# Performance work log

Measured on AMD Instinct MI355X. Metric: run time of the kernel, lower is better.

## Reference

```python
import jax, jax.numpy as jnp
import numpy as np

H = 128      # hidden_sizes
E = 128      # embedding_size
V = 100000   # n_words
C = 10       # n_classes
B, S, L = 32, 32, 64
PAD = 0


def _gru_dir(x, w_ih, w_hh, b_ih, b_hh, reverse):
    # x: [N, T, D]; torch GRU cell convention (r, z, n gate order)
    xp = jnp.einsum('ntd,gd->ntg', x, w_ih) + b_ih  # [N, T, 3H]
    if reverse:
        xp = xp[:, ::-1]
    h0 = jnp.zeros((x.shape[0], w_hh.shape[1]), x.dtype)

    def step(h, xt):
        gh = h @ w_hh.T + b_hh
        xr, xz, xn = jnp.split(xt, 3, axis=-1)
        hr, hz, hn = jnp.split(gh, 3, axis=-1)
        r = jax.nn.sigmoid(xr + hr)
        z = jax.nn.sigmoid(xz + hz)
        n = jnp.tanh(xn + r * hn)
        h2 = (1.0 - z) * n + z * h
        return h2, h2

    _, hs = jax.lax.scan(step, h0, jnp.swapaxes(xp, 0, 1))
    hs = jnp.swapaxes(hs, 0, 1)  # [N, T, H]
    if reverse:
        hs = hs[:, ::-1]
    return hs


def _bi_gru(x, pf, pb):
    return jnp.concatenate([_gru_dir(x, *pf, False), _gru_dir(x, *pb, True)], axis=-1)


def _attn_pool(h, W, b, ctx):
    # h: [N, T, 2H] -> pooled [N, 2H]
    u = jnp.tanh(jnp.einsum('ntd,ed->nte', h, W) + b)
    a = jax.nn.softmax(u @ ctx, axis=1)          # [N, T]
    return jnp.einsum('ntd,nt->nd', h, a)


def setup_inputs() -> dict:
    key = jax.random.key(0)
    ks = jax.random.split(key, 24)
    sc = 0.05
    d = {}
    d['X'] = jax.random.randint(ks[0], (B, S, L), 0, V, dtype=jnp.int32)
    d['emb'] = jax.random.normal(ks[1], (V, E), jnp.float32) * sc
    # word-level bi-GRU (input E)
    d['w_ih_f'] = jax.random.normal(ks[2], (3 * H, E), jnp.float32) * sc
    d['w_hh_f'] = jax.random.normal(ks[3], (3 * H, H), jnp.float32) * sc
    d['b_ih_f'] = jnp.zeros((3 * H,), jnp.float32)
    d['b_hh_f'] = jnp.zeros((3 * H,), jnp.float32)
    d['w_ih_b'] = jax.random.normal(ks[4], (3 * H, E), jnp.float32) * sc
    d['w_hh_b'] = jax.random.normal(ks[5], (3 * H, H), jnp.float32) * sc
    d['b_ih_b'] = jnp.zeros((3 * H,), jnp.float32)
    d['b_hh_b'] = jnp.zeros((3 * H,), jnp.float32)
    d['Ww'] = jax.random.normal(ks[6], (2 * H, 2 * H), jnp.float32) * sc
    d['bw'] = jnp.zeros((2 * H,), jnp.float32)
    d['ctx_w'] = jax.random.normal(ks[7], (2 * H,), jnp.float32) * sc
    # sentence-level bi-GRU (input 2H)
    d['s_ih_f'] = jax.random.normal(ks[8], (3 * H, 2 * H), jnp.float32) * sc
    d['s_hh_f'] = jax.random.normal(ks[9], (3 * H, H), jnp.float32) * sc
    d['sb_ih_f'] = jnp.zeros((3 * H,), jnp.float32)
    d['sb_hh_f'] = jnp.zeros((3 * H,), jnp.float32)
    d['s_ih_b'] = jax.random.normal(ks[10], (3 * H, 2 * H), jnp.float32) * sc
    d['s_hh_b'] = jax.random.normal(ks[11], (3 * H, H), jnp.float32) * sc
    d['sb_ih_b'] = jnp.zeros((3 * H,), jnp.float32)
    d['sb_hh_b'] = jnp.zeros((3 * H,), jnp.float32)
    d['Ws'] = jax.random.normal(ks[12], (2 * H, 2 * H), jnp.float32) * sc
    d['bs'] = jnp.zeros((2 * H,), jnp.float32)
    d['ctx_s'] = jax.random.normal(ks[13], (2 * H,), jnp.float32) * sc
    d['Wc'] = jax.random.normal(ks[14], (C, 2 * H), jnp.float32) * sc
    d['bc'] = jnp.zeros((C,), jnp.float32)
    return d


def reference(X, emb, w_ih_f, w_hh_f, b_ih_f, b_hh_f, w_ih_b, w_hh_b, b_ih_b, b_hh_b,
              Ww, bw, ctx_w, s_ih_f, s_hh_f, sb_ih_f, sb_hh_f, s_ih_b, s_hh_b,
              sb_ih_b, sb_hh_b, Ws, bs, ctx_s, Wc, bc):
    emb = emb.at[PAD].set(0.0)               # padding_idx semantics
    words = emb[X.reshape(B * S, L)]          # [B*S, L, E]
    h_w = _bi_gru(words, (w_ih_f, w_hh_f, b_ih_f, b_hh_f),
                  (w_ih_b, w_hh_b, b_ih_b, b_hh_b))  # [B*S, L, 2H]
    sents = _attn_pool(h_w, Ww, bw, ctx_w).reshape(B, S, 2 * H)
    h_s = _bi_gru(sents, (s_ih_f, s_hh_f, sb_ih_f, sb_hh_f),
                  (s_ih_b, s_hh_b, sb_ih_b, sb_hh_b))  # [B, S, 2H]
    doc = _attn_pool(h_s, Ws, bs, ctx_s)      # [B, 2H]
    return doc @ Wc.T + bc                    # [B, C]
```

## Files before the change

### kernel.cpp

```cpp
#include <hip/hip_runtime.h>
#include <hip/hip_bf16.h>
#include <math.h>

#define Bd 32
#define Sd 32
#define Ld 64
#define Ed 128
#define Hd 128
#define MW 65536
#define MS 1024

#define OFF_WIHT_S   0
#define OFF_WFW_W    196608
#define OFF_WFW_S    262144
#define OFF_W6       327680
#define OFF_BIH_W    622592
#define OFF_BIH_S    623360
#define OFF_BHH_W    624128
#define OFF_BHH_S    624896
#define OFF_WFX      625664
#define OFF_HW       723968
#define OFF_SENTS    17763328
#define OFF_XP_S     18025472
#define OFF_HS       18811904
#define OFF_DOC      19078144
#define OFF_WFHH     19086336
#define WS_FLOATS    19184640

typedef __attribute__((ext_vector_type(8))) short sh8;
typedef __attribute__((ext_vector_type(4))) float f32x4;
typedef unsigned short u16;
typedef unsigned int u32;

#define GLD  388
#define XPLD 385
#define HPLD 520

__device__ __forceinline__ void barrier_lds_only() {
    asm volatile("s_waitcnt lgkmcnt(0)\n\ts_barrier" ::: "memory");
}

__device__ __forceinline__ float sigmoidf_(float x) {
    return __fdividef(1.0f, 1.0f + __expf(-x));
}
__device__ __forceinline__ float tanhf_(float x) {
    float t = __expf(-2.0f * fabsf(x));
    float r = __fdividef(1.0f - t, 1.0f + t);
    return copysignf(r, x);
}
__device__ __forceinline__ u16 bf16_hi(float f) {
    u32 x = __float_as_uint(f);
    return (u16)((x + 0x7fffu + ((x >> 16) & 1u)) >> 16);
}
__device__ __forceinline__ float bf16_f(u16 u) { return __uint_as_float(((u32)u) << 16); }
__device__ __forceinline__ void bf16_split(float f, u16& hi, u16& lo) {
    hi = bf16_hi(f);
    lo = bf16_hi(f - bf16_f(hi));
}

__global__ void prep_all(const float* __restrict__ s_ih_f, const float* __restrict__ s_ih_b,
                         const float* __restrict__ w_ih_f, const float* __restrict__ w_ih_b,
                         const float* __restrict__ w_hh_f, const float* __restrict__ w_hh_b,
                         const float* __restrict__ s_hh_f, const float* __restrict__ s_hh_b,
                         const float* __restrict__ b_ih_f, const float* __restrict__ b_ih_b,
                         const float* __restrict__ sb_ih_f, const float* __restrict__ sb_ih_b,
                         const float* __restrict__ b_hh_f, const float* __restrict__ b_hh_b,
                         const float* __restrict__ sb_hh_f, const float* __restrict__ sb_hh_b,
                         const float* __restrict__ Ww, const float* __restrict__ Ws,
                         float* __restrict__ ws)
{
    const int b = blockIdx.x;
    if (b < 1164) {
        int i = b * 256 + threadIdx.x;
        if (i < 294912) {
            int set = i / 49152;
            if (set < 4) return;
            int rem = i % 49152;
            int k4 = rem / 1536, r2 = rem % 1536, g = r2 >> 2, sub = r2 & 3;
            const float* w = (set==4) ? s_hh_f : s_hh_b;
            ws[OFF_W6 + i] = w[g*128 + k4*4 + sub];
            return;
        }
        i -= 294912;
        if (i < 768) { ws[OFF_BIH_W + i] = (i<384) ? b_ih_f[i] : b_ih_b[i-384]; return; }
        i -= 768;
        if (i < 768) { ws[OFF_BIH_S + i] = (i<384) ? sb_ih_f[i] : sb_ih_b[i-384]; return; }
        i -= 768;
        if (i < 768) { ws[OFF_BHH_W + i] = (i<384) ? b_hh_f[i] : b_hh_b[i-384]; return; }
        i -= 768;
        if (i < 768) { ws[OFF_BHH_S + i] = (i<384) ? sb_hh_f[i] : sb_hh_b[i-384]; return; }
        return;
    }
    if (b < 1932) {
        u16* WFo = (u16*)(ws + OFF_WFHH);
        int i = (b - 1164) * 256 + threadIdx.x;
        int within = i % 49152;
        int combo  = i / 49152;
        int half = combo & 1, dir = combo >> 1;
        int nt  = within / 2048;
        int r2  = within % 2048;
        int q   = r2 >> 9;
        int r3  = r2 & 511;
        int l   = r3 >> 3, e = r3 & 7;
        int n = nt*16 + (l & 15);
        int k = q*32 + ((l >> 4) << 3) + e;
        const float* src = dir ? w_hh_b : w_hh_f;
        float v = src[n*128 + k];
        u16 hi = bf16_hi(v);
        WFo[i] = half ? bf16_hi(v - bf16_f(hi)) : hi;
        return;
    }
    if (b < 3724) {
        u16* WFW_W = (u16*)(ws + OFF_WFW_W);
        u16* WFW_S = (u16*)(ws + OFF_WFW_S);
        u16* WFX   = (u16*)(ws + OFF_WFX);
        int i = (b - 1932) * 256 + threadIdx.x;
        if (i < 262144) {
            int which = i / 131072;
            int w = i % 131072;
            int half = w / 65536;
            int r = w % 65536;
            int nt = r / 4096;
            int r2 = r % 4096;
            int q = r2 / 512;
            int l = (r2 % 512) >> 3, e = r2 & 7;
            int n = nt*16 + (l & 15);
            int k = q*32 + ((l >> 4) << 3) + e;
            const float* src = which ? Ws : Ww;
            float v = src[n*256 + k];
            u16 hi = bf16_hi(v);
            u16 o = half ? bf16_hi(v - bf16_f(hi)) : hi;
            (which ? WFW_S : WFW_W)[w] = o;
            return;
        }
        i -= 262144;
        if (i < 196608) {
            int w = i % 98304;
            int dir = i / 98304;
            int half = w / 49152;
            int r = w % 49152;
            int nt = r / 2048;
            int r2 = r % 2048;
            int q = r2 / 512;
            int l = (r2 % 512) >> 3, e = r2 & 7;
            int n = nt*16 + (l & 15);
            int k = q*32 + ((l >> 4) << 3) + e;
            const float* src = dir ? w_ih_b : w_ih_f;
            float v = src[n*128 + k];
            u16 hi = bf16_hi(v);
            WFX[i] = half ? bf16_hi(v - bf16_f(hi)) : hi;
            return;
        }
        return;
    }
    {
        u16* WFIHS = (u16*)(ws + OFF_W6);
        int i = (b - 3724) * 256 + threadIdx.x;
        int dir  = i / 196608;
        int w    = i % 196608;
        int half = w / 98304;
        int r    = w % 98304;
        int nt = r / 4096;
        int r2 = r % 4096;
        int q  = r2 / 512;
        int l  = (r2 % 512) >> 3, e = r2 & 7;
        int n = nt*16 + (l & 15);
        int k = q*32 + ((l >> 4) << 3) + e;
        const float* src = dir ? s_ih_b : s_ih_f;
        float v = src[n*256 + k];
        u16 hi = bf16_hi(v);
        WFIHS[i] = half ? bf16_hi(v - bf16_f(hi)) : hi;
    }
}

__global__ __launch_bounds__(768)
void gru_word_full(const int* __restrict__ X, const float* __restrict__ emb,
                   const u16* __restrict__ WFX, const u16* __restrict__ WFHH,
                   const float* __restrict__ b_ih_f, const float* __restrict__ b_ih_b,
                   const float* __restrict__ b_hh_f, const float* __restrict__ b_hh_b,
                   u16* __restrict__ houtp)
{
    const int bx = blockIdx.x;
    const int dir = bx >> 7;
    const int blk = bx & 127;
    const int seq0 = blk * 8;
    const int tid = threadIdx.x;
    const int lane = tid & 63;
    const int wid = tid >> 6;

    __shared__ float xp_lds[64 * XPLD];
    __shared__ f32x4 uni4[2048];
    __shared__ u16 h_pk[4 * HPLD];
    __shared__ int ids_s[8][64];
    float* G = (float*)uni4;
    u16* a_pk = (u16*)uni4;

    const int j = tid & 127;
    const int sg = tid >> 7;
    const bool gthread = tid < 512;
    const float* bih = dir ? b_ih_b : b_ih_f;
    const float* bhh = dir ? b_hh_b : b_hh_f;
    float bhr = 0.f, bhz = 0.f, bhn = 0.f;
    if (gthread) { bhr = bhh[j]; bhz = bhh[128 + j]; bhn = bhh[256 + j]; }

    const u16* WXbase = WFX + (long)dir * 98304;
    const u16* WHbase = WFHH + (long)dir * 98304;
    const int nt0 = wid*2, nt1 = wid*2 + 1;
    const int c0 = nt0*16 + (lane & 15);
    const int c1 = nt1*16 + (lane & 15);
    const int qj = j >> 5, subkj = (j >> 3) & 3, ej = j & 7;

    for (int i = tid; i < 512; i += 768)
        ids_s[i >> 6][i & 63] = X[(long)(seq0 + (i >> 6))*64 + (i & 63)];
    for (int i = tid; i < 4*HPLD; i += 768) h_pk[i] = 0;
    __syncthreads();

    float hprev0 = 0.f, hprev1 = 0.f;
    for (int c = 0; c < 8; ++c) {
        asm volatile("" ::: "memory");
        sh8 xh0[4], xl0[4], xh1[4], xl1[4];
#pragma unroll
        for (int q = 0; q < 4; ++q) {
            xh0[q] = *(const sh8*)(WXbase + (nt0*4 + q)*512 + lane*8);
            xl0[q] = *(const sh8*)(WXbase + 49152 + (nt0*4 + q)*512 + lane*8);
            xh1[q] = *(const sh8*)(WXbase + (nt1*4 + q)*512 + lane*8);
            xl1[q] = *(const sh8*)(WXbase + 49152 + (nt1*4 + q)*512 + lane*8);
        }
        const float bv0 = bih[c0], bv1 = bih[c1];
        for (int idx = tid; idx < 2048; idx += 768) {
            int cc2 = idx & 1, rm = (idx >> 1) & 7, subk = (idx >> 4) & 3;
            int q = (idx >> 6) & 3, mfs = idx >> 8;
            int ts = c*8 + rm;
            int t = dir ? 63 - ts : ts;
            int kk = q*32 + subk*8 + cc2*4;
            int id = ids_s[mfs][t];
            float4 v = make_float4(0.f, 0.f, 0.f, 0.f);
            if (id != 0) v = *(const float4*)&emb[(long)id*128 + kk];
            u16 h0,l0,h1,l1,h2,l2,h3,l3;
            bf16_split(v.x,h0,l0); bf16_split(v.y,h1,l1);
            bf16_split(v.z,h2,l2); bf16_split(v.w,h3,l3);
            int lh = subk*16 + rm;
            int base = (mfs*4 + q)*512 + lh*8 + cc2*4;
            uint2 whi = make_uint2((u32)h0 | ((u32)h1 << 16), (u32)h2 | ((u32)h3 << 16));
            uint2 wlo = make_uint2((u32)l0 | ((u32)l1 << 16), (u32)l2 | ((u32)l3 << 16));
            *(uint2*)&a_pk[base]      = whi;
            *(uint2*)&a_pk[base + 64] = wlo;
        }
        barrier_lds_only();
#pragma unroll
        for (int mf = 0; mf < 8; ++mf) {
            f32x4 A0 = (f32x4){0.f,0.f,0.f,0.f};
            f32x4 A1 = (f32x4){0.f,0.f,0.f,0.f};
#pragma unroll
            for (int q = 0; q < 4; ++q) {
                sh8 a = *(const sh8*)&a_pk[(mf*4 + q)*512 + lane*8];
                A0 = __builtin_amdgcn_mfma_f32_16x16x32_bf16(a, xh0[q], A0, 0,0,0);
                A0 = __builtin_amdgcn_mfma_f32_16x16x32_bf16(a, xl0[q], A0, 0,0,0);
                A1 = __builtin_amdgcn_mfma_f32_16x16x32_bf16(a, xh1[q], A1, 0,0,0);
                A1 = __builtin_amdgcn_mfma_f32_16x16x32_bf16(a, xl1[q], A1, 0,0,0);
            }
            float g0[4], g1[4];
#pragma unroll
            for (int r = 0; r < 4; ++r) {
                g0[r] = A0[r] + __shfl_xor(A0[r], 32);
                g1[r] = A1[r] + __shfl_xor(A1[r], 32);
            }
            if ((lane >= 32) == (mf & 1)) {
                int row = mf*8 + ((lane >> 4) & 1)*4;
#pragma unroll
                for (int r = 0; r < 4; ++r) {
                    xp_lds[(row+r)*XPLD + c0] = g0[r] + bv0;
                    xp_lds[(row+r)*XPLD + c1] = g1[r] + bv1;
                }
            }
        }
        barrier_lds_only();
        asm volatile("" ::: "memory");
        sh8 wh0[4], wl0[4], wh1[4], wl1[4];
#pragma unroll
        for (int q = 0; q < 4; ++q) {
            wh0[q] = *(const sh8*)(WHbase + (nt0*4 + q)*512 + lane*8);
            wl0[q] = *(const sh8*)(WHbase + 49152 + (nt0*4 + q)*512 + lane*8);
            wh1[q] = *(const sh8*)(WHbase + (nt1*4 + q)*512 + lane*8);
            wl1[q] = *(const sh8*)(WHbase + 49152 + (nt1*4 + q)*512 + lane*8);
        }
        for (int tt = 0; tt < 8; ++tt) {
            const int ts = c*8 + tt;
            const int t = dir ? 63 - ts : ts;
            f32x4 acc0 = (f32x4){0.f,0.f,0.f,0.f};
            f32x4 acc1 = (f32x4){0.f,0.f,0.f,0.f};
#pragma unroll
            for (int q = 0; q < 4; ++q) {
                sh8 hp = *(const sh8*)&h_pk[q*HPLD + lane*8];
                acc0 = __builtin_amdgcn_mfma_f32_16x16x32_bf16(hp, wh0[q], acc0, 0,0,0);
                acc0 = __builtin_amdgcn_mfma_f32_16x16x32_bf16(hp, wl0[q], acc0, 0,0,0);
                acc1 = __builtin_amdgcn_mfma_f32_16x16x32_bf16(hp, wh1[q], acc1, 0,0,0);
                acc1 = __builtin_amdgcn_mfma_f32_16x16x32_bf16(hp, wl1[q], acc1, 0,0,0);
            }
            {
                float sg0[4], sg1[4];
#pragma unroll
                for (int r = 0; r < 4; ++r) {
                    sg0[r] = acc0[r] + __shfl_xor(acc0[r], 32);
                    sg1[r] = acc1[r] + __shfl_xor(acc1[r], 32);
                }
                if (lane < 32) {
                    const int col16 = lane & 15;
                    const int row0  = (lane >> 4) << 2;
#pragma unroll
                    for (int r = 0; r < 4; ++r) {
                        G[(row0+r)*GLD + nt0*16 + col16] = sg0[r];
                        G[(row0+r)*GLD + nt1*16 + col16] = sg1[r];
                    }
                }
            }
            barrier_lds_only();
            if (gthread) {
#pragma unroll
                for (int si = 0; si < 2; ++si) {
                    const int s = sg + si*4;
                    float gr  = G[s*GLD + j]       + bhr;
                    float gz  = G[s*GLD + 128 + j] + bhz;
                    float gnh = G[s*GLD + 256 + j] + bhn;
                    const float* xrow = &xp_lds[(s*8 + tt)*XPLD];
                    float r  = sigmoidf_(xrow[j] + gr);
                    float z  = sigmoidf_(xrow[128 + j] + gz);
                    float nv = tanhf_(xrow[256 + j] + r * gnh);
                    float hold = si ? hprev1 : hprev0;
                    float hnew = (1.f - z) * nv + z * hold;
                    if (si) hprev1 = hnew; else hprev0 = hnew;
                    u16 hh, hl; bf16_split(hnew, hh, hl);
                    u16 ohh = (u16)__shfl_xor((int)hh, 1);
                    u16 ohl = (u16)__shfl_xor((int)hl, 1);
                    const long tbase = ((long)(seq0 + s)*64 + t)*512 + dir*128;
                    if ((j & 1) == 0) {
                        u32 w = (u32)hh | ((u32)ohh << 16);
                        *(u32*)&h_pk[qj*HPLD + (subkj*16 + s)*8 + ej] = w;
                        *(u32*)&houtp[tbase + j] = w;
                    } else {
                        u32 w = (u32)ohl | ((u32)hl << 16);
                        *(u32*)&h_pk[qj*HPLD + (subkj*16 + s + 8)*8 + (ej - 1)] = w;
                        *(u32*)&houtp[tbase + 256 + (j - 1)] = w;
                    }
                }
            }
            barrier_lds_only();
        }
    }
}

template<int T, bool PACKED, bool CLS>
__global__ __launch_bounds__(1024)
void attn_fused(const float* __restrict__ A, const u16* __restrict__ WF,
                const float* __restrict__ bias, const float* __restrict__ ctx,
                float* __restrict__ outp,
                const float* __restrict__ Wc, const float* __restrict__ bc)
{
    __shared__ u16 a_pk[8][8][512];
    __shared__ float pscore[8][8][17];
    __shared__ float aw[64];
    __shared__ float red[4][256];
    __shared__ float docv[2][256];
    const int tid = threadIdx.x;
    const int lane = tid & 63;
    const int wid = tid >> 6;
    const int m0 = blockIdx.x * 64;

    sh8 bh[8], bl[8];
#pragma unroll
    for (int q = 0; q < 8; ++q) {
        bh[q] = *(const sh8*)(WF + (wid*8 + q)*512 + lane*8);
        bl[q] = *(const sh8*)(WF + 65536 + (wid*8 + q)*512 + lane*8);
    }
    const int colg = wid*16 + (lane & 15);
    const float bwv = bias[colg];
    const float cxv = ctx[colg];

    if (PACKED) {
        const u32* src32 = (const u32*)A + (long)blockIdx.x * 16384;
        u32* dst = (u32*)a_pk;
        for (int idx4 = tid; idx4 < 4096; idx4 += 1024) {
            int idx = idx4 << 2;
            int mf = idx >> 11, q = (idx >> 8) & 7, l = (idx >> 2) & 63;
            int row16 = l & 15, hilo = row16 >> 3, rm = row16 & 7;
            int t = mf*8 + rm;
            int kb2 = q*16 + (l >> 4)*4;
            *(uint4*)&dst[idx] = *(const uint4*)&src32[(t*2 + hilo)*128 + kb2];
        }
    } else {
        for (int idx = tid; idx < 8192; idx += 1024) {
            int row = idx >> 7;
            int k   = (idx & 127) << 1;
            float2 v = *(const float2*)&A[(long)(m0 + row)*256 + k];
            u16 h0,l0,h1,l1; bf16_split(v.x,h0,l0); bf16_split(v.y,h1,l1);
            int mf = row >> 3, rm = row & 7;
            int q = k >> 5;
            int lh = (((k & 31) >> 3) << 4) | rm;
            int e = k & 7;
            *(u32*)&a_pk[mf][q][lh*8 + e]     = (u32)h0 | ((u32)h1 << 16);
            *(u32*)&a_pk[mf][q][(lh+8)*8 + e] = (u32)l0 | ((u32)l1 << 16);
        }
    }
    __syncthreads();

#pragma unroll
    for (int mf = 0; mf < 8; ++mf) {
        f32x4 acc = (f32x4){0.f,0.f,0.f,0.f};
#pragma unroll
        for (int q = 0; q < 8; ++q) {
            sh8 a = *(const sh8*)&a_pk[mf][q][lane*8];
            acc = __builtin_amdgcn_mfma_f32_16x16x32_bf16(a, bh[q], acc, 0,0,0);
            acc = __builtin_amdgcn_mfma_f32_16x16x32_bf16(a, bl[q], acc, 0,0,0);
        }
        float g[4];
#pragma unroll
        for (int r = 0; r < 4; ++r) g[r] = acc[r] + __shfl_xor(acc[r], 32);
        if ((lane >= 32) == (mf & 1)) {
            float p[4];
#pragma unroll
            for (int r = 0; r < 4; ++r) p[r] = tanhf_(g[r] + bwv) * cxv;
#pragma unroll
            for (int r = 0; r < 4; ++r) {
                p[r] += __shfl_xor(p[r], 1);
                p[r] += __shfl_xor(p[r], 2);
                p[r] += __shfl_xor(p[r], 4);
                p[r] += __shfl_xor(p[r], 8);
            }
            if ((lane & 15) == 0) {
#pragma unroll
                for (int r = 0; r < 4; ++r)
                    pscore[mf][((lane >> 4) & 1)*4 + r][wid] = p[r];
            }
        }
    }
    __syncthreads();

    if (tid < 64) {
        float sc = 0.f;
#pragma unroll
        for (int w = 0; w < 16; ++w) sc += pscore[tid >> 3][tid & 7][w];
        float mx = sc;
#pragma unroll
        for (int m = 1; m < T; m <<= 1) mx = fmaxf(mx, __shfl_xor(mx, m));
        float e = __expf(sc - mx);
        float den = e;
#pragma unroll
        for (int m = 1; m < T; m <<= 1) den += __shfl_xor(den, m);
        aw[tid] = __fdividef(e, den);
    }
    __syncthreads();

    if (tid < 512) {
        const int dp = (tid & 127) << 1;
        const int tg = tid >> 7;
        const int q = dp >> 5, lhb = ((dp & 31) >> 3) << 4, e = dp & 7;
        float acc0 = 0.f, acc1 = 0.f;
#pragma unroll
        for (int i = 0; i < 16; ++i) {
            int t = tg*16 + i;
            int mf = t >> 3, rm = t & 7;
            const u16* base = &a_pk[mf][q][(lhb | rm)*8 + e];
            u32 hh = *(const u32*)base;
            u32 ll = *(const u32*)(base + 64);
            float h0 = bf16_f((u16)hh) + bf16_f((u16)ll);
            float h1 = bf16_f((u16)(hh >> 16)) + bf16_f((u16)(ll >> 16));
            float w = aw[t];
            acc0 = fmaf(w, h0, acc0);
            acc1 = fmaf(w, h1, acc1);
        }
        red[tg][dp] = acc0; red[tg][dp + 1] = acc1;
    }
    __syncthreads();
    if (T == 64) {
        if (tid < 256)
            outp[(long)blockIdx.x*256 + tid] = red[0][tid] + red[1][tid] + red[2][tid] + red[3][tid];
    } else if (!CLS) {
        if (tid < 512) {
            int sent = tid >> 8, dd = tid & 255;
            outp[((long)blockIdx.x*2 + sent)*256 + dd] = red[sent*2][dd] + red[sent*2 + 1][dd];
        }
    } else {
        if (tid < 512) {
            int sent = tid >> 8, dd = tid & 255;
            docv[sent][dd] = red[sent*2][dd] + red[sent*2 + 1][dd];
        }
        __syncthreads();
        if (tid < 20) {
            int s = tid / 10, c = tid % 10;
            float acc = bc[c];
            const float4* wp = (const float4*)&Wc[c*256];
            const float4* dv = (const float4*)&docv[s][0];
#pragma unroll 8
            for (int d = 0; d < 64; ++d) {
                float4 a = dv[d], w = wp[d];
                acc = fmaf(a.x, w.x, fmaf(a.y, w.y, fmaf(a.z, w.z, fmaf(a.w, w.w, acc))));
            }
            outp[(blockIdx.x*2 + s)*10 + c] = acc;
        }
    }
}

__global__ __launch_bounds__(512)
void gru_sent(const float* __restrict__ sents, const u16* __restrict__ WFIHS,
              const float* __restrict__ bih_s, const float4* __restrict__ whh4,
              const float* __restrict__ bhh, float* __restrict__ hout)
{
    const int bx = blockIdx.x;
    const int dir = bx >> 5;
    const int doc = bx & 31;
    const int tid = threadIdx.x;
    const int lane = tid & 63;
    const int wid = tid >> 6;

    __shared__ float xp_lds[32 * XPLD];
    __shared__ u16 a_pk[4 * 8 * 512];
    __shared__ float h_lds[128];

    for (int i = tid; i < 128; i += 512) h_lds[i] = 0.f;

    for (int idx = tid; idx < 2048; idx += 512) {
        int cc2 = idx & 1, rm = (idx >> 1) & 7, subk = (idx >> 4) & 3;
        int q = (idx >> 6) & 7, mf = (idx >> 9) & 3;
        int t = mf*8 + rm;
        int kk = q*32 + subk*8 + cc2*4;
        float4 v = *(const float4*)&sents[(long)(doc*32 + t)*256 + kk];
        u16 h0,l0,h1,l1,h2,l2,h3,l3;
        bf16_split(v.x,h0,l0); bf16_split(v.y,h1,l1);
        bf16_split(v.z,h2,l2); bf16_split(v.w,h3,l3);
        int lh = subk*16 + rm;
        int base = (mf*8 + q)*512 + lh*8 + cc2*4;
        uint2 whi = make_uint2((u32)h0 | ((u32)h1 << 16), (u32)h2 | ((u32)h3 << 16));
        uint2 wlo = make_uint2((u32)l0 | ((u32)l1 << 16), (u32)l2 | ((u32)l3 << 16));
        *(uint2*)&a_pk[base]      = whi;
        *(uint2*)&a_pk[base + 64] = wlo;
    }
    barrier_lds_only();

    const u16* WFbase = WFIHS + (long)dir * 196608;
#pragma unroll 1
    for (int ni = 0; ni < 3; ++ni) {
        const int nt = wid + ni*8;
        sh8 wh[8], wl[8];
#pragma unroll
        for (int q = 0; q < 8; ++q) {
            wh[q] = *(const sh8*)(WFbase + (nt*8 + q)*512 + lane*8);
            wl[q] = *(const sh8*)(WFbase + 98304 + (nt*8 + q)*512 + lane*8);
        }
        const int col16 = lane & 15;
        const float bv = bih_s[dir*384 + nt*16 + col16];
        f32x4 A0 = (f32x4){0.f,0.f,0.f,0.f};
        f32x4 A1 = (f32x4){0.f,0.f,0.f,0.f};
        f32x4 A2 = (f32x4){0.f,0.f,0.f,0.f};
        f32x4 A3 = (f32x4){0.f,0.f,0.f,0.f};
#pragma unroll
        for (int q = 0; q < 8; ++q) {
            sh8 a0 = *(const sh8*)&a_pk[(0*8 + q)*512 + lane*8];
            sh8 a1 = *(const sh8*)&a_pk[(1*8 + q)*512 + lane*8];
            sh8 a2 = *(const sh8*)&a_pk[(2*8 + q)*512 + lane*8];
            sh8 a3 = *(const sh8*)&a_pk[(3*8 + q)*512 + lane*8];
            A0 = __builtin_amdgcn_mfma_f32_16x16x32_bf16(a0, wh[q], A0, 0,0,0);
            A0 = __builtin_amdgcn_mfma_f32_16x16x32_bf16(a0, wl[q], A0, 0,0,0);
            A1 = __builtin_amdgcn_mfma_f32_16x16x32_bf16(a1, wh[q], A1, 0,0,0);
            A1 = __builtin_amdgcn_mfma_f32_16x16x32_bf16(a1, wl[q], A1, 0,0,0);
            A2 = __builtin_amdgcn_mfma_f32_16x16x32_bf16(a2, wh[q], A2, 0,0,0);
            A2 = __builtin_amdgcn_mfma_f32_16x16x32_bf16(a2, wl[q], A2, 0,0,0);
            A3 = __builtin_amdgcn_mfma_f32_16x16x32_bf16(a3, wh[q], A3, 0,0,0);
            A3 = __builtin_amdgcn_mfma_f32_16x16x32_bf16(a3, wl[q], A3, 0,0,0);
        }
#pragma unroll
        for (int mf = 0; mf < 4; ++mf) {
            f32x4 A = (mf==0) ? A0 : (mf==1) ? A1 : (mf==2) ? A2 : A3;
            float g[4];
#pragma unroll
            for (int r = 0; r < 4; ++r) g[r] = A[r] + __shfl_xor(A[r], 32);
            if ((lane >= 32) == (mf & 1)) {
                int row = mf*8 + ((lane >> 4) & 1)*4;
#pragma unroll
                for (int r = 0; r < 4; ++r)
                    xp_lds[(row+r)*XPLD + nt*16 + col16] = g[r] + bv;
            }
        }
    }
    barrier_lds_only();
    asm volatile("" ::: "memory");

    const int kq = tid & 3;
    const int j  = tid >> 2;
    const float4* W = whh4 + (long)dir * 12288;
    const float bhr = bhh[dir*384 + j];
    const float bhz = bhh[dir*384 + 128 + j];
    const float bhn = bhh[dir*384 + 256 + j];
    float4 w0r[8], w1r[8], w2r[8];
#pragma unroll
    for (int ii = 0; ii < 8; ++ii) {
        const int k4 = kq + (ii << 2);
        w0r[ii] = W[k4*384 + j];
        w1r[ii] = W[k4*384 + 128 + j];
        w2r[ii] = W[k4*384 + 256 + j];
    }

    for (int ts = 0; ts < 32; ++ts) {
        const int t = dir ? (31 - ts) : ts;
        float a0 = 0.f, a1 = 0.f, a2 = 0.f;
#pragma unroll
        for (int ii = 0; ii < 8; ++ii) {
            const int k4 = kq + (ii << 2);
            float4 w0 = w0r[ii];
            float4 w1 = w1r[ii];
            float4 w2 = w2r[ii];
            float4 h4 = *(const float4*)&h_lds[k4 << 2];
            a0 = fmaf(w0.x,h4.x, fmaf(w0.y,h4.y, fmaf(w0.z,h4.z, fmaf(w0.w,h4.w, a0))));
            a1 = fmaf(w1.x,h4.x, fmaf(w1.y,h4.y, fmaf(w1.z,h4.z, fmaf(w1.w,h4.w, a1))));
            a2 = fmaf(w2.x,h4.x, fmaf(w2.y,h4.y, fmaf(w2.z,h4.z, fmaf(w2.w,h4.w, a2))));
        }
        a0 += __shfl_xor(a0, 1); a0 += __shfl_xor(a0, 2);
        a1 += __shfl_xor(a1, 1); a1 += __shfl_xor(a1, 2);
        a2 += __shfl_xor(a2, 1); a2 += __shfl_xor(a2, 2);
        __syncthreads();
        if (kq == 0) {
            const float* xr = &xp_lds[t*XPLD];
            float r = sigmoidf_(xr[j]       + a0 + bhr);
            float z = sigmoidf_(xr[128 + j] + a1 + bhz);
            float nv = tanhf_(xr[256 + j] + r * (a2 + bhn));
            float hold = h_lds[j];
            float hnew = (1.f - z) * nv + z * hold;
            h_lds[j] = hnew;
            hout[((long)(doc*32) + t)*256*1 + (long)t*0 + ((long)(doc*32 + t))*0] = 0.f;
        }
        __syncthreads();
        if (kq == 0) {
        }
    }
}

__global__ __launch_bounds__(512)
void gru_sent2(const float* __restrict__ sents, const u16* __restrict__ WFIHS,
               const float* __restrict__ bih_s, const float4* __restrict__ whh4,
               const float* __restrict__ bhh, float* __restrict__ hout)
{
    const int bx = blockIdx.x;
    const int dir = bx >> 5;
    const int doc = bx & 31;
    const int tid = threadIdx.x;
    const int lane = tid & 63;
    const int wid = tid >> 6;

    __shared__ float xp_lds[32 * XPLD];
    __shared__ u16 a_pk[4 * 8 * 512];
    __shared__ float h_lds[128];

    for (int i = tid; i < 128; i += 512) h_lds[i] = 0.f;

    for (int idx = tid; idx < 2048; idx += 512) {
        int cc2 = idx & 1, rm = (idx >> 1) & 7, subk = (idx >> 4) & 3;
        int q = (idx >> 6) & 7, mf = (idx >> 9) & 3;
        int t = mf*8 + rm;
        int kk = q*32 + subk*8 + cc2*4;
        float4 v = *(const float4*)&sents[(long)(doc*32 + t)*256 + kk];
        u16 h0,l0,h1,l1,h2,l2,h3,l3;
        bf16_split(v.x,h0,l0); bf16_split(v.y,h1,l1);
        bf16_split(v.z,h2,l2); bf16_split(v.w,h3,l3);
        int lh = subk*16 + rm;
        int base = (mf*8 + q)*512 + lh*8 + cc2*4;
        uint2 whi = make_uint2((u32)h0 | ((u32)h1 << 16), (u32)h2 | ((u32)h3 << 16));
        uint2 wlo = make_uint2((u32)l0 | ((u32)l1 << 16), (u32)l2 | ((u32)l3 << 16));
        *(uint2*)&a_pk[base]      = whi;
        *(uint2*)&a_pk[base + 64] = wlo;
    }
    barrier_lds_only();

    const u16* WFbase = WFIHS + (long)dir * 196608;
#pragma unroll 1
    for (int ni = 0; ni < 3; ++ni) {
        const int nt = wid + ni*8;
        sh8 wh[8], wl[8];
#pragma unroll
        for (int q = 0; q < 8; ++q) {
            wh[q] = *(const sh8*)(WFbase + (nt*8 + q)*512 + lane*8);
            wl[q] = *(const sh8*)(WFbase + 98304 + (nt*8 + q)*512 + lane*8);
        }
        const int col16 = lane & 15;
        const float bv = bih_s[dir*384 + nt*16 + col16];
        f32x4 A0 = (f32x4){0.f,0.f,0.f,0.f};
        f32x4 A1 = (f32x4){0.f,0.f,0.f,0.f};
        f32x4 A2 = (f32x4){0.f,0.f,0.f,0.f};
        f32x4 A3 = (f32x4){0.f,0.f,0.f,0.f};
#pragma unroll
        for (int q = 0; q < 8; ++q) {
            sh8 a0 = *(const sh8*)&a_pk[(0*8 + q)*512 + lane*8];
            sh8 a1 = *(const sh8*)&a_pk[(1*8 + q)*512 + lane*8];
            sh8 a2 = *(const sh8*)&a_pk[(2*8 + q)*512 + lane*8];
            sh8 a3 = *(const sh8*)&a_pk[(3*8 + q)*512 + lane*8];
            A0 = __builtin_amdgcn_mfma_f32_16x16x32_bf16(a0, wh[q], A0, 0,0,0);
            A0 = __builtin_amdgcn_mfma_f32_16x16x32_bf16(a0, wl[q], A0, 0,0,0);
            A1 = __builtin_amdgcn_mfma_f32_16x16x32_bf16(a1, wh[q], A1, 0,0,0);
            A1 = __builtin_amdgcn_mfma_f32_16x16x32_bf16(a1, wl[q], A1, 0,0,0);
            A2 = __builtin_amdgcn_mfma_f32_16x16x32_bf16(a2, wh[q], A2, 0,0,0);
            A2 = __builtin_amdgcn_mfma_f32_16x16x32_bf16(a2, wl[q], A2, 0,0,0);
            A3 = __builtin_amdgcn_mfma_f32_16x16x32_bf16(a3, wh[q], A3, 0,0,0);
            A3 = __builtin_amdgcn_mfma_f32_16x16x32_bf16(a3, wl[q], A3, 0,0,0);
        }
#pragma unroll
        for (int mf = 0; mf < 4; ++mf) {
            f32x4 A = (mf==0) ? A0 : (mf==1) ? A1 : (mf==2) ? A2 : A3;
            float g[4];
#pragma unroll
            for (int r = 0; r < 4; ++r) g[r] = A[r] + __shfl_xor(A[r], 32);
            if ((lane >= 32) == (mf & 1)) {
                int row = mf*8 + ((lane >> 4) & 1)*4;
#pragma unroll
                for (int r = 0; r < 4; ++r)
                    xp_lds[(row+r)*XPLD + nt*16 + col16] = g[r] + bv;
            }
        }
    }
    barrier_lds_only();
    asm volatile("" ::: "memory");

    const int kq = tid & 3;
    const int j  = tid >> 2;
    const float4* W = whh4 + (long)dir * 12288;
    const float bhr = bhh[dir*384 + j];
    const float bhz = bhh[dir*384 + 128 + j];
    const float bhn = bhh[dir*384 + 256 + j];
    float4 w0r[8], w1r[8], w2r[8];
#pragma unroll
    for (int ii = 0; ii < 8; ++ii) {
        const int k4 = kq + (ii << 2);
        w0r[ii] = W[k4*384 + j];
        w1r[ii] = W[k4*384 + 128 + j];
        w2r[ii] = W[k4*384 + 256 + j];
    }

    for (int ts = 0; ts < 32; ++ts) {
        const int t = dir ? (31 - ts) : ts;
        float a0 = 0.f, a1 = 0.f, a2 = 0.f;
#pragma unroll
        for (int ii = 0; ii < 8; ++ii) {
            const int k4 = kq + (ii << 2);
            float4 w0 = w0r[ii];
            float4 w1 = w1r[ii];
            float4 w2 = w2r[ii];
            float4 h4 = *(const float4*)&h_lds[k4 << 2];
            a0 = fmaf(w0.x,h4.x, fmaf(w0.y,h4.y, fmaf(w0.z,h4.z, fmaf(w0.w,h4.w, a0))));
            a1 = fmaf(w1.x,h4.x, fmaf(w1.y,h4.y, fmaf(w1.z,h4.z, fmaf(w1.w,h4.w, a1))));
            a2 = fmaf(w2.x,h4.x, fmaf(w2.y,h4.y, fmaf(w2.z,h4.z, fmaf(w2.w,h4.w, a2))));
        }
        a0 += __shfl_xor(a0, 1); a0 += __shfl_xor(a0, 2);
        a1 += __shfl_xor(a1, 1); a1 += __shfl_xor(a1, 2);
        a2 += __shfl_xor(a2, 1); a2 += __shfl_xor(a2, 2);
        __syncthreads();
        if (kq == 0) {
            const float* xr = &xp_lds[t*XPLD];
            float r = sigmoidf_(xr[j]       + a0 + bhr);
            float z = sigmoidf_(xr[128 + j] + a1 + bhz);
            float nv = tanhf_(xr[256 + j] + r * (a2 + bhn));
            float hold = h_lds[j];
            float hnew = (1.f - z) * nv + z * hold;
            h_lds[j] = hnew;
            hout[((long)(doc*32 + t))*256 + dir*128 + j] = hnew;
        }
        __syncthreads();
    }
}

extern "C" void kernel_launch(void* const* d_in, const int* in_sizes, int n_in,
                              void* d_out, int out_size, void* d_ws, size_t ws_size,
                              hipStream_t stream) {
    const int*   X       = (const int*)  d_in[0];
    const float* emb     = (const float*)d_in[1];
    const float* w_ih_f  = (const float*)d_in[2];
    const float* w_hh_f  = (const float*)d_in[3];
    const float* b_ih_f  = (const float*)d_in[4];
    const float* b_hh_f  = (const float*)d_in[5];
    const float* w_ih_b  = (const float*)d_in[6];
    const float* w_hh_b  = (const float*)d_in[7];
    const float* b_ih_b  = (const float*)d_in[8];
    const float* b_hh_b  = (const float*)d_in[9];
    const float* Ww      = (const float*)d_in[10];
    const float* bw      = (const float*)d_in[11];
    const float* ctx_w   = (const float*)d_in[12];
    const float* s_ih_f  = (const float*)d_in[13];
    const float* s_hh_f  = (const float*)d_in[14];
    const float* sb_ih_f = (const float*)d_in[15];
    const float* sb_hh_f = (const float*)d_in[16];
    const float* s_ih_b  = (const float*)d_in[17];
    const float* s_hh_b  = (const float*)d_in[18];
    const float* sb_ih_b = (const float*)d_in[19];
    const float* sb_hh_b = (const float*)d_in[20];
    const float* Ws      = (const float*)d_in[21];
    const float* bs      = (const float*)d_in[22];
    const float* ctx_s   = (const float*)d_in[23];
    const float* Wc      = (const float*)d_in[24];
    const float* bc      = (const float*)d_in[25];
    float* ws  = (float*)d_ws;
    float* out = (float*)d_out;

    if (ws_size < (size_t)WS_FLOATS * 4) return;

    prep_all<<<5260, 256, 0, stream>>>(s_ih_f, s_ih_b, w_ih_f, w_ih_b,
                                       w_hh_f, w_hh_b, s_hh_f, s_hh_b,
                                       b_ih_f, b_ih_b, sb_ih_f, sb_ih_b,
                                       b_hh_f, b_hh_b, sb_hh_f, sb_hh_b,
                                       Ww, Ws, ws);

    gru_word_full<<<256, 768, 0, stream>>>(
        X, emb, (const u16*)(ws + OFF_WFX), (const u16*)(ws + OFF_WFHH),
        b_ih_f, b_ih_b, b_hh_f, b_hh_b, (u16*)(ws + OFF_HW));

    attn_fused<64, true, false><<<1024, 1024, 0, stream>>>(
        ws + OFF_HW, (const u16*)(ws + OFF_WFW_W), bw, ctx_w, ws + OFF_SENTS,
        nullptr, nullptr);

    gru_sent2<<<64, 512, 0, stream>>>(
        ws + OFF_SENTS, (const u16*)(ws + OFF_W6), ws + OFF_BIH_S,
        (const float4*)(ws + OFF_W6) + 4*12288, ws + OFF_BHH_S, ws + OFF_HS);

    attn_fused<32, false, true><<<16, 1024, 0, stream>>>(
        ws + OFF_HS, (const u16*)(ws + OFF_WFW_S), bs, ctx_s, out, Wc, bc);
}
```

Measured before the change: 308.7 us.

## Prefetch next chunk's embeddings during recurrence using idle non-gate threads

```diff
diff --git a/kernel.cpp b/kernel.cpp
--- a/kernel.cpp
+++ b/kernel.cpp
@@ -189,11 +189,10 @@
     const int wid = tid >> 6;
 
     __shared__ float xp_lds[64 * XPLD];
-    __shared__ f32x4 uni4[2048];
+    __shared__ u16 a_pk[8 * 4 * 512];
+    __shared__ float G[8 * GLD];
     __shared__ u16 h_pk[4 * HPLD];
     __shared__ int ids_s[8][64];
-    float* G = (float*)uni4;
-    u16* a_pk = (u16*)uni4;
 
     const int j = tid & 127;
     const int sg = tid >> 7;
@@ -215,6 +214,26 @@
     for (int i = tid; i < 4*HPLD; i += 768) h_pk[i] = 0;
     __syncthreads();
 
+    for (int idx = tid; idx < 2048; idx += 768) {
+        int cc2 = idx & 1, rm = (idx >> 1) & 7, subk = (idx >> 4) & 3;
+        int q = (idx >> 6) & 3, mfs = idx >> 8;
+        int t = dir ? 63 - rm : rm;
+        int kk = q*32 + subk*8 + cc2*4;
+        int id = ids_s[mfs][t];
+        float4 v = make_float4(0.f, 0.f, 0.f, 0.f);
+        if (id != 0) v = *(const float4*)&emb[(long)id*128 + kk];
+        u16 h0,l0,h1,l1,h2,l2,h3,l3;
+        bf16_split(v.x,h0,l0); bf16_split(v.y,h1,l1);
+        bf16_split(v.z,h2,l2); bf16_split(v.w,h3,l3);
+        int lh = subk*16 + rm;
+        int base = (mfs*4 + q)*512 + lh*8 + cc2*4;
+        uint2 whi = make_uint2((u32)h0 | ((u32)h1 << 16), (u32)h2 | ((u32)h3 << 16));
+        uint2 wlo = make_uint2((u32)l0 | ((u32)l1 << 16), (u32)l2 | ((u32)l3 << 16));
+        *(uint2*)&a_pk[base]      = whi;
+        *(uint2*)&a_pk[base + 64] = wlo;
+    }
+    __syncthreads();
+
     float hprev0 = 0.f, hprev1 = 0.f;
     for (int c = 0; c < 8; ++c) {
         asm volatile("" ::: "memory");
@@ -227,26 +246,6 @@
             xl1[q] = *(const sh8*)(WXbase + 49152 + (nt1*4 + q)*512 + lane*8);
         }
         const float bv0 = bih[c0], bv1 = bih[c1];
-        for (int idx = tid; idx < 2048; idx += 768) {
-            int cc2 = idx & 1, rm = (idx >> 1) & 7, subk = (idx >> 4) & 3;
-            int q = (idx >> 6) & 3, mfs = idx >> 8;
-            int ts = c*8 + rm;
-            int t = dir ? 63 - ts : ts;
-            int kk = q*32 + subk*8 + cc2*4;
-            int id = ids_s[mfs][t];
-            float4 v = make_float4(0.f, 0.f, 0.f, 0.f);
-            if (id != 0) v = *(const float4*)&emb[(long)id*128 + kk];
-            u16 h0,l0,h1,l1,h2,l2,h3,l3;
-            bf16_split(v.x,h0,l0); bf16_split(v.y,h1,l1);
-            bf16_split(v.z,h2,l2); bf16_split(v.w,h3,l3);
-            int lh = subk*16 + rm;
-            int base = (mfs*4 + q)*512 + lh*8 + cc2*4;
-            uint2 whi = make_uint2((u32)h0 | ((u32)h1 << 16), (u32)h2 | ((u32)h3 << 16));
-            uint2 wlo = make_uint2((u32)l0 | ((u32)l1 << 16), (u32)l2 | ((u32)l3 << 16));
-            *(uint2*)&a_pk[base]      = whi;
-            *(uint2*)&a_pk[base + 64] = wlo;
-        }
-        barrier_lds_only();
 #pragma unroll
         for (int mf = 0; mf < 8; ++mf) {
             f32x4 A0 = (f32x4){0.f,0.f,0.f,0.f};
@@ -287,6 +286,23 @@
         for (int tt = 0; tt < 8; ++tt) {
             const int ts = c*8 + tt;
             const int t = dir ? 63 - ts : ts;
+            float4 sv;
+            int s_base = 0;
+            const bool sv_ok = !gthread && (c < 7);
+            if (sv_ok) {
+                const int st = tid - 512;
+                const int idx = tt*256 + st;
+                int cc2 = idx & 1, rm = (idx >> 1) & 7, subk = (idx >> 4) & 3;
+                int q = (idx >> 6) & 3, mfs = idx >> 8;
+                int ts2 = (c+1)*8 + rm;
+                int t2 = dir ? 63 - ts2 : ts2;
+                int kk = q*32 + subk*8 + cc2*4;
+                int id = ids_s[mfs][t2];
+                sv = make_float4(0.f, 0.f, 0.f, 0.f);
+                if (id != 0) sv = *(const float4*)&emb[(long)id*128 + kk];
+                int lh = subk*16 + rm;
+                s_base = (mfs*4 + q)*512 + lh*8 + cc2*4;
+            }
             f32x4 acc0 = (f32x4){0.f,0.f,0.f,0.f};
             f32x4 acc1 = (f32x4){0.f,0.f,0.f,0.f};
 #pragma unroll
@@ -343,6 +359,14 @@
                         *(u32*)&houtp[tbase + 256 + (j - 1)] = w;
                     }
                 }
+            } else if (sv_ok) {
+                u16 h0,l0,h1,l1,h2,l2,h3,l3;
+                bf16_split(sv.x,h0,l0); bf16_split(sv.y,h1,l1);
+                bf16_split(sv.z,h2,l2); bf16_split(sv.w,h3,l3);
+                uint2 whi = make_uint2((u32)h0 | ((u32)h1 << 16), (u32)h2 | ((u32)h3 << 16));
+                uint2 wlo = make_uint2((u32)l0 | ((u32)l1 << 16), (u32)l2 | ((u32)l3 << 16));
+                *(uint2*)&a_pk[s_base]      = whi;
+                *(uint2*)&a_pk[s_base + 64] = wlo;
             }
             barrier_lds_only();
         }
@@ -504,139 +528,6 @@
 void gru_sent(const float* __restrict__ sents, const u16* __restrict__ WFIHS,
               const float* __restrict__ bih_s, const float4* __restrict__ whh4,
               const float* __restrict__ bhh, float* __restrict__ hout)
-{
-    const int bx = blockIdx.x;
-    const int dir = bx >> 5;
-    const int doc = bx & 31;
-    const int tid = threadIdx.x;
-    const int lane = tid & 63;
-    const int wid = tid >> 6;
-
-    __shared__ float xp_lds[32 * XPLD];
-    __shared__ u16 a_pk[4 * 8 * 512];
-    __shared__ float h_lds[128];
-
-    for (int i = tid; i < 128; i += 512) h_lds[i] = 0.f;
-
-    for (int idx = tid; idx < 2048; idx += 512) {
-        int cc2 = idx & 1, rm = (idx >> 1) & 7, subk = (idx >> 4) & 3;
-        int q = (idx >> 6) & 7, mf = (idx >> 9) & 3;
-        int t = mf*8 + rm;
-        int kk = q*32 + subk*8 + cc2*4;
-        float4 v = *(const float4*)&sents[(long)(doc*32 + t)*256 + kk];
-        u16 h0,l0,h1,l1,h2,l2,h3,l3;
-        bf16_split(v.x,h0,l0); bf16_split(v.y,h1,l1);
-        bf16_split(v.z,h2,l2); bf16_split(v.w,h3,l3);
-        int lh = subk*16 + rm;
-        int base = (mf*8 + q)*512 + lh*8 + cc2*4;
-        uint2 whi = make_uint2((u32)h0 | ((u32)h1 << 16), (u32)h2 | ((u32)h3 << 16));
-        uint2 wlo = make_uint2((u32)l0 | ((u32)l1 << 16), (u32)l2 | ((u32)l3 << 16));
-        *(uint2*)&a_pk[base]      = whi;
-        *(uint2*)&a_pk[base + 64] = wlo;
-    }
-    barrier_lds_only();
-
-    const u16* WFbase = WFIHS + (long)dir * 196608;
-#pragma unroll 1
-    for (int ni = 0; ni < 3; ++ni) {
-        const int nt = wid + ni*8;
-        sh8 wh[8], wl[8];
-#pragma unroll
-        for (int q = 0; q < 8; ++q) {
-            wh[q] = *(const sh8*)(WFbase + (nt*8 + q)*512 + lane*8);
-            wl[q] = *(const sh8*)(WFbase + 98304 + (nt*8 + q)*512 + lane*8);
-        }
-        const int col16 = lane & 15;
-        const float bv = bih_s[dir*384 + nt*16 + col16];
-        f32x4 A0 = (f32x4){0.f,0.f,0.f,0.f};
-        f32x4 A1 = (f32x4){0.f,0.f,0.f,0.f};
-        f32x4 A2 = (f32x4){0.f,0.f,0.f,0.f};
-        f32x4 A3 = (f32x4){0.f,0.f,0.f,0.f};
-#pragma unroll
-        for (int q = 0; q < 8; ++q) {
-            sh8 a0 = *(const sh8*)&a_pk[(0*8 + q)*512 + lane*8];
-            sh8 a1 = *(const sh8*)&a_pk[(1*8 + q)*512 + lane*8];
-            sh8 a2 = *(const sh8*)&a_pk[(2*8 + q)*512 + lane*8];
-            sh8 a3 = *(const sh8*)&a_pk[(3*8 + q)*512 + lane*8];
-            A0 = __builtin_amdgcn_mfma_f32_16x16x32_bf16(a0, wh[q], A0, 0,0,0);
-            A0 = __builtin_amdgcn_mfma_f32_16x16x32_bf16(a0, wl[q], A0, 0,0,0);
-            A1 = __builtin_amdgcn_mfma_f32_16x16x32_bf16(a1, wh[q], A1, 0,0,0);
-            A1 = __builtin_amdgcn_mfma_f32_16x16x32_bf16(a1, wl[q], A1, 0,0,0);
-            A2 = __builtin_amdgcn_mfma_f32_16x16x32_bf16(a2, wh[q], A2, 0,0,0);
-            A2 = __builtin_amdgcn_mfma_f32_16x16x32_bf16(a2, wl[q], A2, 0,0,0);
-            A3 = __builtin_amdgcn_mfma_f32_16x16x32_bf16(a3, wh[q], A3, 0,0,0);
-            A3 = __builtin_amdgcn_mfma_f32_16x16x32_bf16(a3, wl[q], A3, 0,0,0);
-        }
-#pragma unroll
-        for (int mf = 0; mf < 4; ++mf) {
-            f32x4 A = (mf==0) ? A0 : (mf==1) ? A1 : (mf==2) ? A2 : A3;
-            float g[4];
-#pragma unroll
-            for (int r = 0; r < 4; ++r) g[r] = A[r] + __shfl_xor(A[r], 32);
-            if ((lane >= 32) == (mf & 1)) {
-                int row = mf*8 + ((lane >> 4) & 1)*4;
-#pragma unroll
-                for (int r = 0; r < 4; ++r)
-                    xp_lds[(row+r)*XPLD + nt*16 + col16] = g[r] + bv;
-            }
-        }
-    }
-    barrier_lds_only();
-    asm volatile("" ::: "memory");
-
-    const int kq = tid & 3;
-    const int j  = tid >> 2;
-    const float4* W = whh4 + (long)dir * 12288;
-    const float bhr = bhh[dir*384 + j];
-    const float bhz = bhh[dir*384 + 128 + j];
-    const float bhn = bhh[dir*384 + 256 + j];
-    float4 w0r[8], w1r[8], w2r[8];
-#pragma unroll
-    for (int ii = 0; ii < 8; ++ii) {
-        const int k4 = kq + (ii << 2);
-        w0r[ii] = W[k4*384 + j];
-        w1r[ii] = W[k4*384 + 128 + j];
-        w2r[ii] = W[k4*384 + 256 + j];
-    }
-
-    for (int ts = 0; ts < 32; ++ts) {
-        const int t = dir ? (31 - ts) : ts;
-        float a0 = 0.f, a1 = 0.f, a2 = 0.f;
-#pragma unroll
-        for (int ii = 0; ii < 8; ++ii) {
-            const int k4 = kq + (ii << 2);
-            float4 w0 = w0r[ii];
-            float4 w1 = w1r[ii];
-            float4 w2 = w2r[ii];
-            float4 h4 = *(const float4*)&h_lds[k4 << 2];
-            a0 = fmaf(w0.x,h4.x, fmaf(w0.y,h4.y, fmaf(w0.z,h4.z, fmaf(w0.w,h4.w, a0))));
-            a1 = fmaf(w1.x,h4.x, fmaf(w1.y,h4.y, fmaf(w1.z,h4.z, fmaf(w1.w,h4.w, a1))));
-            a2 = fmaf(w2.x,h4.x, fmaf(w2.y,h4.y, fmaf(w2.z,h4.z, fmaf(w2.w,h4.w, a2))));
-        }
-        a0 += __shfl_xor(a0, 1); a0 += __shfl_xor(a0, 2);
-        a1 += __shfl_xor(a1, 1); a1 += __shfl_xor(a1, 2);
-        a2 += __shfl_xor(a2, 1); a2 += __shfl_xor(a2, 2);
-        __syncthreads();
-        if (kq == 0) {
-            const float* xr = &xp_lds[t*XPLD];
-            float r = sigmoidf_(xr[j]       + a0 + bhr);
-            float z = sigmoidf_(xr[128 + j] + a1 + bhz);
-            float nv = tanhf_(xr[256 + j] + r * (a2 + bhn));
-            float hold = h_lds[j];
-            float hnew = (1.f - z) * nv + z * hold;
-            h_lds[j] = hnew;
-            hout[((long)(doc*32) + t)*256*1 + (long)t*0 + ((long)(doc*32 + t))*0] = 0.f;
-        }
-        __syncthreads();
-        if (kq == 0) {
-        }
-    }
-}
-
-__global__ __launch_bounds__(512)
-void gru_sent2(const float* __restrict__ sents, const u16* __restrict__ WFIHS,
-               const float* __restrict__ bih_s, const float4* __restrict__ whh4,
-               const float* __restrict__ bhh, float* __restrict__ hout)
 {
     const int bx = blockIdx.x;
     const int dir = bx >> 5;
@@ -812,7 +703,7 @@
         ws + OFF_HW, (const u16*)(ws + OFF_WFW_W), bw, ctx_w, ws + OFF_SENTS,
         nullptr, nullptr);
 
-    gru_sent2<<<64, 512, 0, stream>>>(
+    gru_sent<<<64, 512, 0, stream>>>(
         ws + OFF_SENTS, (const u16*)(ws + OFF_W6), ws + OFF_BIH_S,
         (const float4*)(ws + OFF_W6) + 4*12288, ws + OFF_BHH_S, ws + OFF_HS);
 
```

Result: no change. 307.3 us (-0.5%).
